# Performance work log

Measured on AMD Instinct MI355X. Metric: run time of the kernel, lower is better.

The kernel has to match this reference:

```python
import jax, jax.numpy as jnp
import numpy as np
from jax import lax

HEADS = 16
HEAD_DIM = 64
EPS = 1e-5

def _act_quant(x):
    # per-token int8 absmax quantization (BitNet b1.58)
    scale = 127.0 / jnp.clip(jnp.max(jnp.abs(x), axis=-1, keepdims=True), EPS)
    return jnp.clip(jnp.round(x * scale), -128.0, 127.0) / scale

def _weight_quant(w):
    # ternary weight quantization with mean-absmax scale
    scale = 1.0 / jnp.clip(jnp.mean(jnp.abs(w)), EPS)
    return jnp.clip(jnp.round(w * scale), -1.0, 1.0) / scale

def bitlinear(x, w):
    # straight-through estimator: forward uses quantized, backward sees identity
    xq = x + lax.stop_gradient(_act_quant(x) - x)
    wq = w + lax.stop_gradient(_weight_quant(w) - w)
    return jnp.einsum('bsd,od->bso', xq, wq)

def setup_inputs() -> dict:
    key = jax.random.key(0)
    ks = jax.random.split(key, 5)
    B, S, D = 2, 2048, 1024
    x = jax.random.normal(ks[0], (B, S, D), dtype=jnp.float32)
    # causal mask (B, 1, S, S): 1 = keep, 0 = masked
    mask = jnp.broadcast_to(jnp.tril(jnp.ones((S, S), dtype=jnp.int32))[None, None], (B, 1, S, S))
    scale = 0.02
    Wq = jax.random.normal(ks[1], (D, D), dtype=jnp.float32) * scale
    Wk = jax.random.normal(ks[2], (D, D), dtype=jnp.float32) * scale
    Wv = jax.random.normal(ks[3], (D, D), dtype=jnp.float32) * scale
    Wo = jax.random.normal(ks[4], (D, D), dtype=jnp.float32) * scale
    return {"x": x, "mask": mask, "Wq": Wq, "Wk": Wk, "Wv": Wv, "Wo": Wo}

def reference(x, mask, Wq, Wk, Wv, Wo):
    B, S, D = x.shape
    H, Hd = HEADS, HEAD_DIM
    q = bitlinear(x, Wq).reshape(B, S, H, Hd).transpose(0, 2, 1, 3)  # (B,H,S,Hd)
    k = bitlinear(x, Wk).reshape(B, S, H, Hd).transpose(0, 2, 1, 3)
    v = bitlinear(x, Wv).reshape(B, S, H, Hd).transpose(0, 2, 1, 3)
    attn = jnp.einsum('bhsd,bhtd->bhst', q, k) / jnp.sqrt(jnp.float32(Hd))
    attn = jnp.where(mask == 0, -jnp.inf, attn)
    attn = jax.nn.softmax(attn, axis=-1)
    out = jnp.einsum('bhst,bhtd->bhsd', attn, v)
    out = out.transpose(0, 2, 1, 3).reshape(B, S, D)
    return bitlinear(out, Wo)
```

## Files before the change

### kernel.cpp

```cpp
#include <hip/hip_runtime.h>
#include <hip/hip_bf16.h>
#include <math.h>


typedef float  f32x4  __attribute__((ext_vector_type(4)));
typedef __bf16 bf16x8 __attribute__((ext_vector_type(8)));
typedef unsigned int u32x4 __attribute__((ext_vector_type(4)));

#define EPSV 1e-5f

__device__ __forceinline__ f32x4 mfma16(bf16x8 a, bf16x8 b, f32x4 c) {
    return __builtin_amdgcn_mfma_f32_16x16x32_bf16(a, b, c, 0, 0, 0);
}

__device__ __forceinline__ void gload16(const void* g, void* lds) {
    __builtin_amdgcn_global_load_lds((const __attribute__((address_space(1))) unsigned int*)g,
                                     (__attribute__((address_space(3))) unsigned int*)lds, 16, 0, 0);
}

__global__ __launch_bounds__(256) void k_wsum(const float* __restrict__ w0, const float* __restrict__ w1,
                                              const float* __restrict__ w2, const float* __restrict__ w3,
                                              double* __restrict__ wsum) {
    int w = blockIdx.x >> 6, chunk = blockIdx.x & 63, tid = threadIdx.x;
    const float* W = (w == 0) ? w0 : (w == 1) ? w1 : (w == 2) ? w2 : w3;
    const float* base = W + (size_t)chunk * 16384;
    float s = 0.f;
#pragma unroll
    for (int i = 0; i < 16; i++) {
        f32x4 v = *(const f32x4*)(base + i * 1024 + tid * 4);
        s += fabsf(v.x) + fabsf(v.y) + fabsf(v.z) + fabsf(v.w);
    }
#pragma unroll
    for (int off = 1; off < 64; off <<= 1) s += __shfl_xor(s, off);
    __shared__ float red[4];
    if ((tid & 63) == 0) red[tid >> 6] = s;
    __syncthreads();
    if (tid == 0) {
        double t = (double)red[0] + (double)red[1] + (double)red[2] + (double)red[3];
        atomicAdd(&wsum[w], t);
    }
}

__global__ __launch_bounds__(256) void k_wquant(const float* __restrict__ w0, const float* __restrict__ w1,
                                                const float* __restrict__ w2, const float* __restrict__ w3,
                                                const double* __restrict__ wsum,
                                                __bf16* __restrict__ wq, float* __restrict__ wm) {
    int w = blockIdx.y;
    const float* W = (w == 0) ? w0 : (w == 1) ? w1 : (w == 2) ? w2 : w3;
    float mean = (float)(wsum[w] * (1.0 / 1048576.0));
    float ms = fmaxf(mean, EPSV);
    float scale = 1.0f / ms;
    int pos = blockIdx.x * 1024 + threadIdx.x * 4;
    f32x4 v = *(const f32x4*)(W + pos);
    float q0 = fminf(fmaxf(rintf(v.x * scale), -1.f), 1.f);
    float q1 = fminf(fmaxf(rintf(v.y * scale), -1.f), 1.f);
    float q2 = fminf(fmaxf(rintf(v.z * scale), -1.f), 1.f);
    float q3 = fminf(fmaxf(rintf(v.w * scale), -1.f), 1.f);
    unsigned int b0 = __builtin_bit_cast(unsigned short, (__bf16)q0);
    unsigned int b1 = __builtin_bit_cast(unsigned short, (__bf16)q1);
    unsigned int b2 = __builtin_bit_cast(unsigned short, (__bf16)q2);
    unsigned int b3 = __builtin_bit_cast(unsigned short, (__bf16)q3);
    uint2 p; p.x = b0 | (b1 << 16); p.y = b2 | (b3 << 16);
    *(uint2*)(wq + (size_t)w * 1048576 + pos) = p;
    if (blockIdx.x == 0 && threadIdx.x == 0) wm[w] = ms;
}

__global__ __launch_bounds__(256) void k_actq(const float* __restrict__ in, __bf16* __restrict__ outq,
                                              float* __restrict__ rs) {
    int t = blockIdx.x, tid = threadIdx.x;
    const float* row = in + (size_t)t * 1024;
    f32x4 v = *(const f32x4*)(row + tid * 4);
    float am = fmaxf(fmaxf(fabsf(v.x), fabsf(v.y)), fmaxf(fabsf(v.z), fabsf(v.w)));
#pragma unroll
    for (int off = 1; off < 64; off <<= 1) am = fmaxf(am, __shfl_xor(am, off));
    __shared__ float red[4];
    if ((tid & 63) == 0) red[tid >> 6] = am;
    __syncthreads();
    am = fmaxf(fmaxf(red[0], red[1]), fmaxf(red[2], red[3]));
    am = fmaxf(am, EPSV);
    float scale = 127.0f / am;
    float q0 = fminf(fmaxf(rintf(v.x * scale), -128.f), 127.f);
    float q1 = fminf(fmaxf(rintf(v.y * scale), -128.f), 127.f);
    float q2 = fminf(fmaxf(rintf(v.z * scale), -128.f), 127.f);
    float q3 = fminf(fmaxf(rintf(v.w * scale), -128.f), 127.f);
    unsigned int b0 = __builtin_bit_cast(unsigned short, (__bf16)q0);
    unsigned int b1 = __builtin_bit_cast(unsigned short, (__bf16)q1);
    unsigned int b2 = __builtin_bit_cast(unsigned short, (__bf16)q2);
    unsigned int b3 = __builtin_bit_cast(unsigned short, (__bf16)q3);
    uint2 p; p.x = b0 | (b1 << 16); p.y = b2 | (b3 << 16);
    *(uint2*)(outq + (size_t)t * 1024 + tid * 4) = p;
    if (tid == 0) rs[t] = am / 127.0f;
}

template <int MODE>
__global__ __launch_bounds__(256) void k_gemm(const __bf16* __restrict__ X, const __bf16* __restrict__ Wb,
                                              const float* __restrict__ rs, const float* __restrict__ wm,
                                              __bf16* __restrict__ o0, __bf16* __restrict__ o1,
                                              __bf16* __restrict__ o2, float* __restrict__ outf) {
    __shared__ __attribute__((aligned(16))) __bf16 As[128 * 32];
    __shared__ __attribute__((aligned(16))) __bf16 Bs[128 * 32];
    int tid = threadIdx.x;
    int wave = tid >> 6, lane = tid & 63, g = lane >> 4, l = lane & 15;
    int m0 = blockIdx.x * 128, n0 = blockIdx.y * 128;
    int z = blockIdx.z;
    const __bf16* W = Wb + (size_t)z * 1048576;
    float wmv = wm[z];
    f32x4 acc[4][4] = {};
    int srow0 = wave * 16 + (lane >> 2);
    int scol = (lane & 3) * 8;
    const __bf16* Ag = X + (size_t)(m0 + srow0) * 1024 + scol;
    const __bf16* Bg = W + (size_t)(n0 + srow0) * 1024 + scol;
    __bf16* ldsA = As + wave * 512;
    __bf16* ldsB = Bs + wave * 512;
    int wrow = (wave >> 1) * 64, wcol = (wave & 1) * 64;
    bool vswap = (MODE == 0) && (z == 2);
    for (int k0 = 0; k0 < 1024; k0 += 32) {
        __syncthreads();
        gload16(Ag + k0,             ldsA);
        gload16(Ag + 64 * 1024 + k0, ldsA + 2048);
        gload16(Bg + k0,             ldsB);
        gload16(Bg + 64 * 1024 + k0, ldsB + 2048);
        __syncthreads();
        bf16x8 af[4], bfr[4];
#pragma unroll
        for (int i = 0; i < 4; i++) af[i]  = *(const bf16x8*)&As[(wrow + i * 16 + l) * 32 + 8 * g];
#pragma unroll
        for (int i = 0; i < 4; i++) bfr[i] = *(const bf16x8*)&Bs[(wcol + i * 16 + l) * 32 + 8 * g];
        if (vswap) {
#pragma unroll
            for (int mi = 0; mi < 4; mi++)
#pragma unroll
                for (int ni = 0; ni < 4; ni++)
                    acc[mi][ni] = mfma16(bfr[ni], af[mi], acc[mi][ni]);
        } else {
#pragma unroll
            for (int mi = 0; mi < 4; mi++)
#pragma unroll
                for (int ni = 0; ni < 4; ni++)
                    acc[mi][ni] = mfma16(af[mi], bfr[ni], acc[mi][ni]);
        }
    }
    if (vswap) {
#pragma unroll
        for (int mi = 0; mi < 4; mi++) {
            int m = m0 + wrow + mi * 16 + l;
            float rsm = rs[m] * wmv;
            int b = m >> 11, s2 = m & 2047;
#pragma unroll
            for (int ni = 0; ni < 4; ni++) {
                int nb = n0 + wcol + ni * 16 + 4 * g;
#pragma unroll
                for (int r = 0; r < 4; r++) {
                    int n = nb + r;
                    int h = n >> 6, hd = n & 63;
                    o2[((size_t)(b * 16 + h) * 64 + hd) * 2048 + s2] = (__bf16)(acc[mi][ni][r] * rsm);
                }
            }
        }
        return;
    }
#pragma unroll
    for (int mi = 0; mi < 4; mi++) {
        int mbase = m0 + wrow + mi * 16 + 4 * g;
        f32x4 rv = {rs[mbase], rs[mbase + 1], rs[mbase + 2], rs[mbase + 3]};
#pragma unroll
        for (int ni = 0; ni < 4; ni++) {
            int n = n0 + wcol + ni * 16 + l;
#pragma unroll
            for (int r = 0; r < 4; r++) {
                float v = acc[mi][ni][r] * (rv[r] * wmv);
                if constexpr (MODE == 0) {
                    int m = mbase + r;
                    int b = m >> 11, s2 = m & 2047;
                    int h = n >> 6, hd = n & 63;
                    __bf16* dst = (z == 0) ? o0 : o1;
                    dst[(((size_t)(b * 16 + h)) * 2048 + s2) * 64 + hd] = (__bf16)v;
                } else {
                    outf[(size_t)(mbase + r) * 1024 + n] = v;
                }
            }
        }
    }
}

__global__ __launch_bounds__(512) void k_attn(const __bf16* __restrict__ qg, const __bf16* __restrict__ kb,
                                              const __bf16* __restrict__ vt, float* __restrict__ attn) {
    __shared__ __attribute__((aligned(16))) __bf16 Ks[2][4096];
    __shared__ __attribute__((aligned(16))) __bf16 Vs[2][4096];
    __shared__ __attribute__((aligned(16))) __bf16 Ps[8][1024];
    int tid = threadIdx.x, w = tid >> 6, lane = tid & 63, g = lane >> 4, l = lane & 15;
    int bh = blockIdx.y, bq = bh >> 4, h = bh & 15;
    int q0 = blockIdx.x * 128;
    size_t bhq = (size_t)bh * 2048 * 64;
    int qlo = q0 + w * 16, qmax = qlo + 15;
    int qrow = qlo + l;
    bf16x8 aq0 = *(const bf16x8*)(qg + bhq + (size_t)qrow * 64 + 8 * g);
    bf16x8 aq1 = *(const bf16x8*)(qg + bhq + (size_t)qrow * 64 + 32 + 8 * g);
    f32x4 o[4] = {};
    float mreg[4], lsum[4];
#pragma unroll
    for (int r = 0; r < 4; r++) { mreg[r] = -INFINITY; lsum[r] = 0.f; }
    char* Pw = (char*)&Ps[w][0];
    int psw = (l & 7) << 4;
    int sRow = w * 8 + (lane >> 3);
    int sCol = ((lane & 7) ^ (lane >> 3)) << 3;
    const __bf16* Kg = kb + bhq + (size_t)sRow * 64 + sCol;
    const __bf16* Vg = vt + bhq + (size_t)sRow * 2048 + sCol;
    int nt = 2 * (blockIdx.x + 1);
    gload16(Kg, &Ks[0][w * 512]);
    gload16(Vg, &Vs[0][w * 512]);
    __syncthreads();
    for (int ti = 0; ti < nt; ti++) {
        int t0 = ti * 64;
        int tn = ti + 1;
        if (tn < nt) {
            gload16(Kg + (size_t)tn * 4096, &Ks[tn & 1][w * 512]);
            gload16(Vg + tn * 64,           &Vs[tn & 1][w * 512]);
        }
        if (t0 <= qmax) {
            const char* Kb = (const char*)&Ks[ti & 1][0];
            const char* Vb = (const char*)&Vs[ti & 1][0];
            f32x4 sv[4];
            __builtin_amdgcn_s_setprio(1);
#pragma unroll
            for (int nb = 0; nb < 4; nb++) {
                int kr = nb * 16 + l;
                const char* kbase = Kb + kr * 128;
                int sz = (kr & 7) << 4;
                bf16x8 bk0 = *(const bf16x8*)(kbase + ((16 * g) ^ sz));
                bf16x8 bk1 = *(const bf16x8*)(kbase + ((64 + 16 * g) ^ sz));
                f32x4 a = {};
                a = mfma16(aq0, bk0, a);
                a = mfma16(aq1, bk1, a);
                sv[nb] = a * 0.125f;
            }
            __builtin_amdgcn_s_setprio(0);
            if (t0 + 63 > qlo) {
#pragma unroll
                for (int nb = 0; nb < 4; nb++)
#pragma unroll
                    for (int r = 0; r < 4; r++) {
                        int key = t0 + nb * 16 + l;
                        int q = qlo + 4 * g + r;
                        if (key > q) sv[nb][r] = -INFINITY;
                    }
            }
            float corr[4];
#pragma unroll
            for (int r = 0; r < 4; r++) {
                float v = fmaxf(fmaxf(sv[0][r], sv[1][r]), fmaxf(sv[2][r], sv[3][r]));
                v = fmaxf(v, __shfl_xor(v, 1));
                v = fmaxf(v, __shfl_xor(v, 2));
                v = fmaxf(v, __shfl_xor(v, 4));
                v = fmaxf(v, __shfl_xor(v, 8));
                float mnew = fmaxf(mreg[r], v);
                corr[r] = __expf(mreg[r] - mnew);
                mreg[r] = mnew;
            }
            float ps[4] = {0.f, 0.f, 0.f, 0.f};
#pragma unroll
            for (int nb = 0; nb < 4; nb++)
#pragma unroll
                for (int r = 0; r < 4; r++) {
                    float pe = __expf(sv[nb][r] - mreg[r]);
                    sv[nb][r] = pe;
                    ps[r] += pe;
                }
#pragma unroll
            for (int r = 0; r < 4; r++) {
                float sm = ps[r];
                sm += __shfl_xor(sm, 1);
                sm += __shfl_xor(sm, 2);
                sm += __shfl_xor(sm, 4);
                sm += __shfl_xor(sm, 8);
                lsum[r] = lsum[r] * corr[r] + sm;
#pragma unroll
                for (int hb = 0; hb < 4; hb++) o[hb][r] = o[hb][r] * corr[r];
            }
#pragma unroll
            for (int nb = 0; nb < 4; nb++)
#pragma unroll
                for (int r = 0; r < 4; r++) {
                    int prow = 4 * g + r;
                    *(__bf16*)(Pw + prow * 128 + ((nb * 32 + 2 * l) ^ ((prow & 7) << 4))) = (__bf16)sv[nb][r];
                }
            bf16x8 pa0 = *(const bf16x8*)(Pw + l * 128 + ((16 * g) ^ psw));
            bf16x8 pa1 = *(const bf16x8*)(Pw + l * 128 + ((64 + 16 * g) ^ psw));
            __builtin_amdgcn_s_setprio(1);
#pragma unroll
            for (int hb = 0; hb < 4; hb++) {
                int vr = hb * 16 + l;
                const char* vbase = Vb + vr * 128;
                int sz = (vr & 7) << 4;
                bf16x8 v0 = *(const bf16x8*)(vbase + ((16 * g) ^ sz));
                bf16x8 v1 = *(const bf16x8*)(vbase + ((64 + 16 * g) ^ sz));
                o[hb] = mfma16(pa0, v0, o[hb]);
                o[hb] = mfma16(pa1, v1, o[hb]);
            }
            __builtin_amdgcn_s_setprio(0);
        }
        __syncthreads();
    }
#pragma unroll
    for (int r = 0; r < 4; r++) {
        float inv = 1.0f / lsum[r];
        int q = qlo + 4 * g + r;
        float* dst = attn + ((size_t)(bq * 2048 + q)) * 1024 + h * 64 + l;
#pragma unroll
        for (int hb = 0; hb < 4; hb++) dst[hb * 16] = o[hb][r] * inv;
    }
}

extern "C" void kernel_launch(void* const* d_in, const int* in_sizes, int n_in,
                              void* d_out, int out_size, void* d_ws, size_t ws_size,
                              hipStream_t stream) {
    const float* x  = (const float*)d_in[0];
    const float* Wq = (const float*)d_in[2];
    const float* Wk = (const float*)d_in[3];
    const float* Wv = (const float*)d_in[4];
    const float* Wo = (const float*)d_in[5];
    float* out = (float*)d_out;
    char* ws = (char*)d_ws;

    double* wsumd = (double*)(ws + 0);
    float*  wmv   = (float*)(ws + 256);
    __bf16* wqall = (__bf16*)(ws + 512);
    __bf16* xq    = (__bf16*)(ws + 512 + 8388608);
    float*  rsx   = (float*)(ws + 512 + 16777216);
    float*  rso   = (float*)(ws + 512 + 16777216 + 16384);
    char*   big   = ws + 512 + 16777216 + 32768;
    __bf16* qbuf  = (__bf16*)(big);
    __bf16* kbuf  = (__bf16*)(big + 8388608);
    __bf16* oq    = (__bf16*)(big + 16777216);
    __bf16* vtb   = (__bf16*)(big + 25165824);
    float*  attn  = (float*)(big + 33554432);

    hipMemsetAsync(ws, 0, 512, stream);
    k_wsum<<<dim3(256), 256, 0, stream>>>(Wq, Wk, Wv, Wo, wsumd);
    k_wquant<<<dim3(1024, 4), 256, 0, stream>>>(Wq, Wk, Wv, Wo, wsumd, wqall, wmv);
    k_actq<<<dim3(4096), 256, 0, stream>>>(x, xq, rsx);
    k_gemm<0><<<dim3(32, 8, 3), 256, 0, stream>>>(xq, wqall, rsx, wmv, qbuf, kbuf, vtb, nullptr);
    k_attn<<<dim3(16, 32), 512, 0, stream>>>(qbuf, kbuf, vtb, attn);
    k_actq<<<dim3(4096), 256, 0, stream>>>(attn, oq, rso);
    k_gemm<1><<<dim3(32, 8, 1), 256, 0, stream>>>(oq, wqall + 3 * 1048576, rso, wmv + 3,
                                                  nullptr, nullptr, nullptr, out);
}
```

Baseline: 280.5 us.

## Transpose attention MFMA to keep P in registers and triple-buffer K/V

The QK^T MFMA operands are swapped so each lane holds a full score column per query. Softmax statistics then become per-lane scalars reduced with only two cross-lane shuffles, and the P tile can be packed straight into the PV MFMA operand without a round trip through LDS. K/V staging moves from double to triple buffering with explicit vmcnt waits and a single barrier per iteration, and the output is written as float4 vectors. This removes the per-warp P shared buffer and the second barrier, at the cost of more LDS for K/V and split 8-byte V reads.

```diff
diff --git a/kernel.cpp b/kernel.cpp
--- a/kernel.cpp
+++ b/kernel.cpp
@@ -5,6 +5,7 @@
 
 typedef float  f32x4  __attribute__((ext_vector_type(4)));
 typedef __bf16 bf16x8 __attribute__((ext_vector_type(8)));
+typedef __bf16 bf16x4 __attribute__((ext_vector_type(4)));
 typedef unsigned int u32x4 __attribute__((ext_vector_type(4)));
 
 #define EPSV 1e-5f
@@ -185,9 +186,8 @@
 
 __global__ __launch_bounds__(512) void k_attn(const __bf16* __restrict__ qg, const __bf16* __restrict__ kb,
                                               const __bf16* __restrict__ vt, float* __restrict__ attn) {
-    __shared__ __attribute__((aligned(16))) __bf16 Ks[2][4096];
-    __shared__ __attribute__((aligned(16))) __bf16 Vs[2][4096];
-    __shared__ __attribute__((aligned(16))) __bf16 Ps[8][1024];
+    __shared__ __attribute__((aligned(16))) __bf16 Ks[3][4096];
+    __shared__ __attribute__((aligned(16))) __bf16 Vs[3][4096];
     int tid = threadIdx.x, w = tid >> 6, lane = tid & 63, g = lane >> 4, l = lane & 15;
     int bh = blockIdx.y, bq = bh >> 4, h = bh & 15;
     int q0 = blockIdx.x * 128;
@@ -196,42 +196,45 @@
     int qrow = qlo + l;
     bf16x8 aq0 = *(const bf16x8*)(qg + bhq + (size_t)qrow * 64 + 8 * g);
     bf16x8 aq1 = *(const bf16x8*)(qg + bhq + (size_t)qrow * 64 + 32 + 8 * g);
+    asm volatile("" : "+v"(aq0), "+v"(aq1));
     f32x4 o[4] = {};
-    float mreg[4], lsum[4];
-#pragma unroll
-    for (int r = 0; r < 4; r++) { mreg[r] = -INFINITY; lsum[r] = 0.f; }
-    char* Pw = (char*)&Ps[w][0];
-    int psw = (l & 7) << 4;
+    float mreg = -INFINITY, lsum = 0.f;
     int sRow = w * 8 + (lane >> 3);
     int sCol = ((lane & 7) ^ (lane >> 3)) << 3;
     const __bf16* Kg = kb + bhq + (size_t)sRow * 64 + sCol;
     const __bf16* Vg = vt + bhq + (size_t)sRow * 2048 + sCol;
     int nt = 2 * (blockIdx.x + 1);
-    gload16(Kg, &Ks[0][w * 512]);
-    gload16(Vg, &Vs[0][w * 512]);
-    __syncthreads();
-    for (int ti = 0; ti < nt; ti++) {
-        int t0 = ti * 64;
-        int tn = ti + 1;
+    gload16(Kg,        &Ks[0][w * 512]);
+    gload16(Vg,        &Vs[0][w * 512]);
+    gload16(Kg + 4096, &Ks[1][w * 512]);
+    gload16(Vg + 64,   &Vs[1][w * 512]);
+    int cur = 0;
+    int swk = (l & 7) << 4;
+    for (int t = 0; t < nt; ++t) {
+        if (t < nt - 1) { asm volatile("s_waitcnt vmcnt(2)"); }
+        else            { asm volatile("s_waitcnt vmcnt(0)"); }
+        __builtin_amdgcn_s_barrier();
+        __builtin_amdgcn_sched_barrier(0);
+        int tn = t + 2;
         if (tn < nt) {
-            gload16(Kg + (size_t)tn * 4096, &Ks[tn & 1][w * 512]);
-            gload16(Vg + tn * 64,           &Vs[tn & 1][w * 512]);
-        }
+            int nbuf = cur + 2; if (nbuf >= 3) nbuf -= 3;
+            gload16(Kg + (size_t)tn * 4096, &Ks[nbuf][w * 512]);
+            gload16(Vg + tn * 64,           &Vs[nbuf][w * 512]);
+        }
+        int t0 = t * 64;
         if (t0 <= qmax) {
-            const char* Kb = (const char*)&Ks[ti & 1][0];
-            const char* Vb = (const char*)&Vs[ti & 1][0];
+            const char* Kb = (const char*)&Ks[cur][0];
+            const char* Vb = (const char*)&Vs[cur][0];
             f32x4 sv[4];
             __builtin_amdgcn_s_setprio(1);
 #pragma unroll
             for (int nb = 0; nb < 4; nb++) {
-                int kr = nb * 16 + l;
-                const char* kbase = Kb + kr * 128;
-                int sz = (kr & 7) << 4;
-                bf16x8 bk0 = *(const bf16x8*)(kbase + ((16 * g) ^ sz));
-                bf16x8 bk1 = *(const bf16x8*)(kbase + ((64 + 16 * g) ^ sz));
+                const char* kbase = Kb + (nb * 16 + l) * 128;
+                bf16x8 bk0 = *(const bf16x8*)(kbase + ((16 * g) ^ swk));
+                bf16x8 bk1 = *(const bf16x8*)(kbase + ((64 + 16 * g) ^ swk));
                 f32x4 a = {};
-                a = mfma16(aq0, bk0, a);
-                a = mfma16(aq1, bk1, a);
+                a = mfma16(bk0, aq0, a);
+                a = mfma16(bk1, aq1, a);
                 sv[nb] = a * 0.125f;
             }
             __builtin_amdgcn_s_setprio(0);
@@ -240,74 +243,67 @@
                 for (int nb = 0; nb < 4; nb++)
 #pragma unroll
                     for (int r = 0; r < 4; r++) {
-                        int key = t0 + nb * 16 + l;
-                        int q = qlo + 4 * g + r;
-                        if (key > q) sv[nb][r] = -INFINITY;
+                        int key = t0 + nb * 16 + 4 * g + r;
+                        if (key > qrow) sv[nb][r] = -INFINITY;
                     }
             }
-            float corr[4];
-#pragma unroll
-            for (int r = 0; r < 4; r++) {
-                float v = fmaxf(fmaxf(sv[0][r], sv[1][r]), fmaxf(sv[2][r], sv[3][r]));
-                v = fmaxf(v, __shfl_xor(v, 1));
-                v = fmaxf(v, __shfl_xor(v, 2));
-                v = fmaxf(v, __shfl_xor(v, 4));
-                v = fmaxf(v, __shfl_xor(v, 8));
-                float mnew = fmaxf(mreg[r], v);
-                corr[r] = __expf(mreg[r] - mnew);
-                mreg[r] = mnew;
-            }
-            float ps[4] = {0.f, 0.f, 0.f, 0.f};
+            float pm0 = fmaxf(fmaxf(sv[0][0], sv[0][1]), fmaxf(sv[0][2], sv[0][3]));
+            float pm1 = fmaxf(fmaxf(sv[1][0], sv[1][1]), fmaxf(sv[1][2], sv[1][3]));
+            float pm2 = fmaxf(fmaxf(sv[2][0], sv[2][1]), fmaxf(sv[2][2], sv[2][3]));
+            float pm3 = fmaxf(fmaxf(sv[3][0], sv[3][1]), fmaxf(sv[3][2], sv[3][3]));
+            float pm = fmaxf(fmaxf(pm0, pm1), fmaxf(pm2, pm3));
+            pm = fmaxf(pm, __shfl_xor(pm, 16));
+            pm = fmaxf(pm, __shfl_xor(pm, 32));
+            float mnew = fmaxf(mreg, pm);
+            float corr = __expf(mreg - mnew);
+            mreg = mnew;
+            float psum = 0.f;
 #pragma unroll
             for (int nb = 0; nb < 4; nb++)
 #pragma unroll
                 for (int r = 0; r < 4; r++) {
-                    float pe = __expf(sv[nb][r] - mreg[r]);
+                    float pe = __expf(sv[nb][r] - mnew);
                     sv[nb][r] = pe;
-                    ps[r] += pe;
+                    psum += pe;
                 }
-#pragma unroll
-            for (int r = 0; r < 4; r++) {
-                float sm = ps[r];
-                sm += __shfl_xor(sm, 1);
-                sm += __shfl_xor(sm, 2);
-                sm += __shfl_xor(sm, 4);
-                sm += __shfl_xor(sm, 8);
-                lsum[r] = lsum[r] * corr[r] + sm;
-#pragma unroll
-                for (int hb = 0; hb < 4; hb++) o[hb][r] = o[hb][r] * corr[r];
-            }
-#pragma unroll
-            for (int nb = 0; nb < 4; nb++)
-#pragma unroll
-                for (int r = 0; r < 4; r++) {
-                    int prow = 4 * g + r;
-                    *(__bf16*)(Pw + prow * 128 + ((nb * 32 + 2 * l) ^ ((prow & 7) << 4))) = (__bf16)sv[nb][r];
-                }
-            bf16x8 pa0 = *(const bf16x8*)(Pw + l * 128 + ((16 * g) ^ psw));
-            bf16x8 pa1 = *(const bf16x8*)(Pw + l * 128 + ((64 + 16 * g) ^ psw));
+            psum += __shfl_xor(psum, 16);
+            psum += __shfl_xor(psum, 32);
+            lsum = lsum * corr + psum;
+#pragma unroll
+            for (int hb = 0; hb < 4; hb++) o[hb] *= corr;
+            bf16x8 pf0, pf1;
+#pragma unroll
+            for (int j = 0; j < 8; j++) {
+                pf0[j] = (__bf16)sv[j >> 2][j & 3];
+                pf1[j] = (__bf16)sv[2 + (j >> 2)][j & 3];
+            }
             __builtin_amdgcn_s_setprio(1);
 #pragma unroll
             for (int hb = 0; hb < 4; hb++) {
-                int vr = hb * 16 + l;
-                const char* vbase = Vb + vr * 128;
-                int sz = (vr & 7) << 4;
-                bf16x8 v0 = *(const bf16x8*)(vbase + ((16 * g) ^ sz));
-                bf16x8 v1 = *(const bf16x8*)(vbase + ((64 + 16 * g) ^ sz));
-                o[hb] = mfma16(pa0, v0, o[hb]);
-                o[hb] = mfma16(pa1, v1, o[hb]);
+                int vrow = hb * 16 + l;
+                const char* vb = Vb + vrow * 128;
+                int rsw = vrow & 7;
+                int ib = 8 * (g & 1);
+                int gh = g >> 1;
+                bf16x4 v00 = *(const bf16x4*)(vb + 16 * ((gh + 0) ^ rsw) + ib);
+                bf16x4 v01 = *(const bf16x4*)(vb + 16 * ((gh + 2) ^ rsw) + ib);
+                bf16x8 vf0 = __builtin_shufflevector(v00, v01, 0, 1, 2, 3, 4, 5, 6, 7);
+                o[hb] = mfma16(vf0, pf0, o[hb]);
+                bf16x4 v10 = *(const bf16x4*)(vb + 16 * ((gh + 4) ^ rsw) + ib);
+                bf16x4 v11 = *(const bf16x4*)(vb + 16 * ((gh + 6) ^ rsw) + ib);
+                bf16x8 vf1 = __builtin_shufflevector(v10, v11, 0, 1, 2, 3, 4, 5, 6, 7);
+                o[hb] = mfma16(vf1, pf1, o[hb]);
             }
             __builtin_amdgcn_s_setprio(0);
         }
-        __syncthreads();
-    }
-#pragma unroll
-    for (int r = 0; r < 4; r++) {
-        float inv = 1.0f / lsum[r];
-        int q = qlo + 4 * g + r;
-        float* dst = attn + ((size_t)(bq * 2048 + q)) * 1024 + h * 64 + l;
-#pragma unroll
-        for (int hb = 0; hb < 4; hb++) dst[hb * 16] = o[hb][r] * inv;
+        cur = (cur + 1 == 3) ? 0 : cur + 1;
+    }
+    float inv = 1.0f / lsum;
+    float* dst = attn + ((size_t)(bq * 2048 + qlo + l)) * 1024 + h * 64 + 4 * g;
+#pragma unroll
+    for (int hb = 0; hb < 4; hb++) {
+        f32x4 vsto = o[hb] * inv;
+        *(f32x4*)(dst + 16 * hb) = vsto;
     }
 }
 
```

Measured after the change: 254.1 us. 1.1x faster.
